# Performance work log

Hardware: AMD Instinct MI355X
Metric: run time of the kernel (lower is better)

The kernel has to match this reference:

```python
import jax, jax.numpy as jnp
import numpy as np

D_MODEL = 1024
D_FF = 4 * D_MODEL
NUM_TILES = 8
B, T = 4, 2048


def setup_inputs() -> dict:
    key = jax.random.key(0)
    ks = jax.random.split(key, 7)
    s = 0.02
    return {
        "x": jax.random.normal(ks[0], (B, T, D_MODEL), dtype=jnp.float32),
        "gate_W": jax.random.normal(ks[1], (D_MODEL, NUM_TILES), dtype=jnp.float32) * s,
        "gate_b": jnp.zeros((NUM_TILES,), dtype=jnp.float32),
        "up_W": jax.random.normal(ks[2], (NUM_TILES, D_MODEL, D_FF), dtype=jnp.float32) * s,
        "up_b": jnp.zeros((NUM_TILES, D_FF), dtype=jnp.float32),
        "down_W": jax.random.normal(ks[3], (NUM_TILES, D_FF, D_MODEL), dtype=jnp.float32) * s,
        "down_b": jnp.zeros((NUM_TILES, D_MODEL), dtype=jnp.float32),
    }


def top1_gate(logits):
    # Hard one-hot of argmax; straight-through identity gradient (Top1Gate).
    hard = jax.nn.one_hot(jnp.argmax(logits, axis=-1), logits.shape[-1], dtype=logits.dtype)
    return hard + (logits - jax.lax.stop_gradient(logits))


def trix_linear(x, gate, W, b):
    # x: [N, I], gate: [N, E] one-hot, W: [E, I, O], b: [E, O]
    # Per-tile linear combined by gate weight; loop over small fixed E.
    out = jnp.zeros((x.shape[0], W.shape[2]), dtype=x.dtype)
    for e in range(W.shape[0]):
        out = out + gate[:, e:e + 1] * (x @ W[e] + b[e])
    return out


def reference(x, gate_W, gate_b, up_W, up_b, down_W, down_b):
    Bv, Tv, C = x.shape
    xf = x.reshape(Bv * Tv, C)                      # [N, C]
    gate = top1_gate(xf @ gate_W + gate_b)          # [N, E]
    h = jax.nn.relu(trix_linear(xf, gate, up_W, up_b))   # [N, 4C]
    # dropout in eval mode (identity)
    out = trix_linear(h, gate, down_W, down_b)      # [N, C]
    return out.reshape(Bv, Tv, C), gate.reshape(Bv, Tv, -1)
```

## Files before the change

### kernel.cpp

```cpp
#include <hip/hip_runtime.h>
#include <hip/hip_bf16.h>
#include <stdint.h>

#define NTOK 8192
#define DM   1024
#define DFF  4096
#define NE   8

typedef __bf16 bf16x8 __attribute__((ext_vector_type(8)));
typedef short  short8 __attribute__((ext_vector_type(8)));
typedef float  floatx4 __attribute__((ext_vector_type(4)));

#define WS_CNT   0
#define WS_OFF   64
#define WS_EIDX  1024
#define WS_PERM  (WS_EIDX + NTOK * 4)
#define WS_XPERM (WS_PERM + NTOK * 4)
#define WS_HPERM (WS_XPERM + (NTOK + 128) * DM * 2)

__device__ __forceinline__ unsigned short f2bf(float f) {
  union { float f; unsigned u; } v; v.f = f;
  return (unsigned short)((v.u + 0x7FFFu + ((v.u >> 16) & 1u)) >> 16);
}

__device__ __forceinline__ float f4get(const float4& v, int i) {
  return i == 0 ? v.x : i == 1 ? v.y : i == 2 ? v.z : v.w;
}

__global__ __launch_bounds__(256) void gate_kernel(
    const float* __restrict__ x, const float* __restrict__ gW,
    const float* __restrict__ gb, float* __restrict__ gate_out,
    int* __restrict__ eidx) {
  int wave = threadIdx.x >> 6;
  int lane = threadIdx.x & 63;
  int t = blockIdx.x * 4 + wave;
  const float4* xr = (const float4*)(x + (size_t)t * DM + lane * 16);
  float acc[8] = {0, 0, 0, 0, 0, 0, 0, 0};
#pragma unroll
  for (int q = 0; q < 4; ++q) {
    float4 xv = xr[q];
    int kbase = lane * 16 + q * 4;
#pragma unroll
    for (int d = 0; d < 4; ++d) {
      float xs = f4get(xv, d);
      const float4* g4 = (const float4*)(gW + (size_t)(kbase + d) * NE);
      float4 g0 = g4[0], g1 = g4[1];
      acc[0] += xs * g0.x; acc[1] += xs * g0.y;
      acc[2] += xs * g0.z; acc[3] += xs * g0.w;
      acc[4] += xs * g1.x; acc[5] += xs * g1.y;
      acc[6] += xs * g1.z; acc[7] += xs * g1.w;
    }
  }
#pragma unroll
  for (int off = 32; off > 0; off >>= 1) {
#pragma unroll
    for (int e = 0; e < 8; ++e) acc[e] += __shfl_down(acc[e], off);
  }
  if (lane == 0) {
    float best = acc[0] + gb[0];
    int bi = 0;
#pragma unroll
    for (int e = 1; e < 8; ++e) {
      float v = acc[e] + gb[e];
      if (v > best) { best = v; bi = e; }
    }
#pragma unroll
    for (int e = 0; e < 8; ++e) gate_out[(size_t)t * NE + e] = (e == bi) ? 1.0f : 0.0f;
    eidx[t] = bi;
  }
}

__global__ __launch_bounds__(1024) void rank_kernel(
    const int* __restrict__ eidx, int* __restrict__ counts,
    int* __restrict__ offs, int* __restrict__ perm) {
  __shared__ unsigned long long sa[1024], sb[1024];
  int tid = threadIdx.x;
  int e8[8];
  unsigned long long ca = 0, cb = 0;
#pragma unroll
  for (int j = 0; j < 8; ++j) {
    int e = eidx[tid * 8 + j];
    e8[j] = e;
    if (e < 4) ca += 1ull << (16 * e);
    else       cb += 1ull << (16 * (e - 4));
  }
  sa[tid] = ca; sb[tid] = cb;
  __syncthreads();
  for (int off = 1; off < 1024; off <<= 1) {
    unsigned long long ta = 0, tb = 0;
    if (tid >= off) { ta = sa[tid - off]; tb = sb[tid - off]; }
    __syncthreads();
    sa[tid] += ta; sb[tid] += tb;
    __syncthreads();
  }
  unsigned long long tot_a = sa[1023], tot_b = sb[1023];
  int cnt_e[8];
#pragma unroll
  for (int e = 0; e < 4; ++e) cnt_e[e] = (int)((tot_a >> (16 * e)) & 0xFFFF);
#pragma unroll
  for (int e = 0; e < 4; ++e) cnt_e[e + 4] = (int)((tot_b >> (16 * e)) & 0xFFFF);
  int off_e[8]; int s = 0;
#pragma unroll
  for (int e = 0; e < 8; ++e) { off_e[e] = s; s += cnt_e[e]; }
  if (tid < 8) { counts[tid] = cnt_e[tid]; offs[tid] = off_e[tid]; }
  unsigned long long ia = sa[tid] - ca, ib = sb[tid] - cb;
  int run[8];
#pragma unroll
  for (int e = 0; e < 4; ++e) run[e] = (int)((ia >> (16 * e)) & 0xFFFF);
#pragma unroll
  for (int e = 0; e < 4; ++e) run[e + 4] = (int)((ib >> (16 * e)) & 0xFFFF);
#pragma unroll
  for (int j = 0; j < 8; ++j) {
    int e = e8[j];
    int pos = off_e[e] + run[e]++;
    perm[pos] = tid * 8 + j;
  }
}

__global__ __launch_bounds__(256) void scatter_data_kernel(
    const float* __restrict__ x, const int* __restrict__ perm,
    unsigned short* __restrict__ xperm) {
  int wave = threadIdx.x >> 6, lane = threadIdx.x & 63;
  int p = blockIdx.x * 4 + wave;
  int t = perm[p];
  const float4* xr = (const float4*)(x + (size_t)t * DM);
#pragma unroll
  for (int q = 0; q < 4; ++q) {
    float4 v = xr[q * 64 + lane];
    uint2 pk;
    pk.x = (unsigned)f2bf(v.x) | ((unsigned)f2bf(v.y) << 16);
    pk.y = (unsigned)f2bf(v.z) | ((unsigned)f2bf(v.w) << 16);
    *(uint2*)(xperm + (size_t)p * DM + q * 256 + lane * 4) = pk;
  }
}

__global__ __launch_bounds__(256) void up_gemm_kernel(
    const unsigned short* __restrict__ xperm,
    const float* __restrict__ upW, const float* __restrict__ upB,
    const int* __restrict__ counts, const int* __restrict__ offs,
    unsigned short* __restrict__ hperm) {
  int e = blockIdx.y >> 6;
  int mt = blockIdx.y & 63;
  int cnt = counts[e];
  if (mt * 128 >= cnt) return;
  int row0 = offs[e] + mt * 128;
  int rows_valid = cnt - mt * 128; if (rows_valid > 128) rows_valid = 128;
  int n0 = blockIdx.x * 128;
  const float* Bg = upW + (size_t)e * DM * DFF;

  __shared__ unsigned short sA[128 * 40];
  __shared__ unsigned short sB[128 * 40];

  int tid = threadIdx.x;
  int wave = tid >> 6, lane = tid & 63;
  int wm = (wave >> 1) * 64, wn = (wave & 1) * 64;

  floatx4 acc[4][4];
#pragma unroll
  for (int i = 0; i < 4; ++i)
#pragma unroll
    for (int j = 0; j < 4; ++j) acc[i][j] = (floatx4){0.f, 0.f, 0.f, 0.f};

  int ar = tid >> 2;
  int ac = (tid & 3) * 8;
  int nq = (tid & 31) * 4;
  int kq = (tid >> 5) * 4;

  for (int k0 = 0; k0 < DM; k0 += 32) {
    __syncthreads();
#pragma unroll
    for (int p = 0; p < 2; ++p) {
      int r = p * 64 + ar;
      short8 av = *(const short8*)(xperm + (size_t)(row0 + r) * DM + k0 + ac);
      *(short8*)(sA + r * 40 + ac) = av;
    }
    float4 bv[4];
#pragma unroll
    for (int dk = 0; dk < 4; ++dk)
      bv[dk] = *(const float4*)(Bg + (size_t)(k0 + kq + dk) * DFF + n0 + nq);
#pragma unroll
    for (int dn = 0; dn < 4; ++dn) {
      uint2 pk;
      pk.x = (unsigned)f2bf(f4get(bv[0], dn)) | ((unsigned)f2bf(f4get(bv[1], dn)) << 16);
      pk.y = (unsigned)f2bf(f4get(bv[2], dn)) | ((unsigned)f2bf(f4get(bv[3], dn)) << 16);
      *(uint2*)(sB + (nq + dn) * 40 + kq) = pk;
    }
    __syncthreads();
    bf16x8 a[4], b[4];
#pragma unroll
    for (int i = 0; i < 4; ++i)
      a[i] = *(const bf16x8*)(sA + (wm + i * 16 + (lane & 15)) * 40 + (lane >> 4) * 8);
#pragma unroll
    for (int j = 0; j < 4; ++j)
      b[j] = *(const bf16x8*)(sB + (wn + j * 16 + (lane & 15)) * 40 + (lane >> 4) * 8);
#pragma unroll
    for (int i = 0; i < 4; ++i)
#pragma unroll
      for (int j = 0; j < 4; ++j)
        acc[i][j] = __builtin_amdgcn_mfma_f32_16x16x32_bf16(a[i], b[j], acc[i][j], 0, 0, 0);
  }

  const float* ub = upB + (size_t)e * DFF;
#pragma unroll
  for (int i = 0; i < 4; ++i) {
#pragma unroll
    for (int r = 0; r < 4; ++r) {
      int rl = wm + i * 16 + (lane >> 4) * 4 + r;
      if (rl < rows_valid) {
        size_t rowg = (size_t)(row0 + rl) * DFF;
#pragma unroll
        for (int j = 0; j < 4; ++j) {
          int col = n0 + wn + j * 16 + (lane & 15);
          float v = acc[i][j][r] + ub[col];
          v = v > 0.f ? v : 0.f;
          hperm[rowg + col] = f2bf(v);
        }
      }
    }
  }
}

__global__ __launch_bounds__(256) void down_gemm_kernel(
    const unsigned short* __restrict__ hperm,
    const float* __restrict__ dW, const float* __restrict__ dB,
    const int* __restrict__ counts, const int* __restrict__ offs,
    const int* __restrict__ perm, float* __restrict__ out) {
  int e = blockIdx.y >> 6;
  int mt = blockIdx.y & 63;
  int cnt = counts[e];
  if (mt * 128 >= cnt) return;
  int row0 = offs[e] + mt * 128;
  int rows_valid = cnt - mt * 128; if (rows_valid > 128) rows_valid = 128;
  int n0 = blockIdx.x * 128;
  const float* Bg = dW + (size_t)e * DFF * DM;

  __shared__ unsigned short sA[128 * 40];
  __shared__ unsigned short sB[128 * 40];

  int tid = threadIdx.x;
  int wave = tid >> 6, lane = tid & 63;
  int wm = (wave >> 1) * 64, wn = (wave & 1) * 64;

  floatx4 acc[4][4];
#pragma unroll
  for (int i = 0; i < 4; ++i)
#pragma unroll
    for (int j = 0; j < 4; ++j) acc[i][j] = (floatx4){0.f, 0.f, 0.f, 0.f};

  int ar = tid >> 2;
  int ac = (tid & 3) * 8;
  int nq = (tid & 31) * 4;
  int kq = (tid >> 5) * 4;

  for (int k0 = 0; k0 < DFF; k0 += 32) {
    __syncthreads();
#pragma unroll
    for (int p = 0; p < 2; ++p) {
      int r = p * 64 + ar;
      short8 av = *(const short8*)(hperm + (size_t)(row0 + r) * DFF + k0 + ac);
      *(short8*)(sA + r * 40 + ac) = av;
    }
    float4 bv[4];
#pragma unroll
    for (int dk = 0; dk < 4; ++dk)
      bv[dk] = *(const float4*)(Bg + (size_t)(k0 + kq + dk) * DM + n0 + nq);
#pragma unroll
    for (int dn = 0; dn < 4; ++dn) {
      uint2 pk;
      pk.x = (unsigned)f2bf(f4get(bv[0], dn)) | ((unsigned)f2bf(f4get(bv[1], dn)) << 16);
      pk.y = (unsigned)f2bf(f4get(bv[2], dn)) | ((unsigned)f2bf(f4get(bv[3], dn)) << 16);
      *(uint2*)(sB + (nq + dn) * 40 + kq) = pk;
    }
    __syncthreads();
    bf16x8 a[4], b[4];
#pragma unroll
    for (int i = 0; i < 4; ++i)
      a[i] = *(const bf16x8*)(sA + (wm + i * 16 + (lane & 15)) * 40 + (lane >> 4) * 8);
#pragma unroll
    for (int j = 0; j < 4; ++j)
      b[j] = *(const bf16x8*)(sB + (wn + j * 16 + (lane & 15)) * 40 + (lane >> 4) * 8);
#pragma unroll
    for (int i = 0; i < 4; ++i)
#pragma unroll
      for (int j = 0; j < 4; ++j)
        acc[i][j] = __builtin_amdgcn_mfma_f32_16x16x32_bf16(a[i], b[j], acc[i][j], 0, 0, 0);
  }

  const float* db = dB + (size_t)e * DM;
#pragma unroll
  for (int i = 0; i < 4; ++i) {
#pragma unroll
    for (int r = 0; r < 4; ++r) {
      int rl = wm + i * 16 + (lane >> 4) * 4 + r;
      if (rl < rows_valid) {
        int token = perm[row0 + rl];
        size_t og = (size_t)token * DM;
#pragma unroll
        for (int j = 0; j < 4; ++j) {
          int col = n0 + wn + j * 16 + (lane & 15);
          out[og + col] = acc[i][j][r] + db[col];
        }
      }
    }
  }
}

extern "C" void kernel_launch(void* const* d_in, const int* in_sizes, int n_in,
                              void* d_out, int out_size, void* d_ws, size_t ws_size,
                              hipStream_t stream) {
  const float* x   = (const float*)d_in[0];
  const float* gW  = (const float*)d_in[1];
  const float* gb  = (const float*)d_in[2];
  const float* upW = (const float*)d_in[3];
  const float* upB = (const float*)d_in[4];
  const float* dW  = (const float*)d_in[5];
  const float* dB  = (const float*)d_in[6];
  float* out      = (float*)d_out;
  float* gate_out = out + (size_t)NTOK * DM;

  char* ws = (char*)d_ws;
  int* cnt  = (int*)(ws + WS_CNT);
  int* off  = (int*)(ws + WS_OFF);
  int* eidx = (int*)(ws + WS_EIDX);
  int* perm = (int*)(ws + WS_PERM);
  unsigned short* xperm = (unsigned short*)(ws + WS_XPERM);
  unsigned short* hperm = (unsigned short*)(ws + WS_HPERM);

  gate_kernel<<<NTOK / 4, 256, 0, stream>>>(x, gW, gb, gate_out, eidx);
  rank_kernel<<<1, 1024, 0, stream>>>(eidx, cnt, off, perm);
  scatter_data_kernel<<<NTOK / 4, 256, 0, stream>>>(x, perm, xperm);
  up_gemm_kernel<<<dim3(DFF / 128, NE * 64), 256, 0, stream>>>(xperm, upW, upB, cnt, off, hperm);
  down_gemm_kernel<<<dim3(DM / 128, NE * 64), 256, 0, stream>>>(hperm, dW, dB, cnt, off, perm, out);
}
```

Before: 671.4 us.

## Pre-convert weights to transposed bf16 and use direct global-to-LDS loads

Adds a conversion kernel that casts the up and down weights to bf16 once per call and transposes them to K-contiguous layout in workspace. The GEMMs then fill shared memory with global_load_lds 16-byte transfers instead of loading fp32 and converting in registers, and drop the padded LDS stride. A 1D grid remap interleaves workgroups across XCDs. This adds a full weight read and write pass each call, and the unpadded LDS layout may cause bank conflicts on the MFMA operand reads.

```diff
diff --git a/kernel.cpp b/kernel.cpp
--- a/kernel.cpp
+++ b/kernel.cpp
@@ -16,7 +16,9 @@
 #define WS_EIDX  1024
 #define WS_PERM  (WS_EIDX + NTOK * 4)
 #define WS_XPERM (WS_PERM + NTOK * 4)
-#define WS_HPERM (WS_XPERM + (NTOK + 128) * DM * 2)
+#define WS_HPERM (WS_XPERM + (size_t)(NTOK + 128) * DM * 2)
+#define WS_UPWT  (WS_HPERM + (size_t)(NTOK + 128) * DFF * 2)
+#define WS_DWT   (WS_UPWT + (size_t)NE * DM * DFF * 2)
 
 __device__ __forceinline__ unsigned short f2bf(float f) {
   union { float f; unsigned u; } v; v.f = f;
@@ -25,6 +27,38 @@
 
 __device__ __forceinline__ float f4get(const float4& v, int i) {
   return i == 0 ? v.x : i == 1 ? v.y : i == 2 ? v.z : v.w;
+}
+
+__device__ __forceinline__ void gload_lds16(const void* g, void* l) {
+  __builtin_amdgcn_global_load_lds(
+      (const __attribute__((address_space(1))) unsigned int*)g,
+      (__attribute__((address_space(3))) unsigned int*)l, 16, 0, 0);
+}
+
+__global__ __launch_bounds__(256) void wconv_kernel(
+    const float* __restrict__ W, unsigned short* __restrict__ Wt,
+    int K, int N) {
+  __shared__ __attribute__((aligned(16))) unsigned short s[64][72];
+  int n0 = blockIdx.x * 64;
+  int k0 = blockIdx.y * 64;
+  const float* Wp = W + (size_t)blockIdx.z * K * N + (size_t)k0 * N + n0;
+  int t = threadIdx.x;
+  int kr = t >> 4;
+  int nc = (t & 15) * 4;
+#pragma unroll
+  for (int q = 0; q < 4; ++q) {
+    float4 v = *(const float4*)(Wp + (size_t)(q * 16 + kr) * N + nc);
+    s[nc + 0][q * 16 + kr] = f2bf(v.x);
+    s[nc + 1][q * 16 + kr] = f2bf(v.y);
+    s[nc + 2][q * 16 + kr] = f2bf(v.z);
+    s[nc + 3][q * 16 + kr] = f2bf(v.w);
+  }
+  __syncthreads();
+  int nr = t >> 2;
+  int kc = (t & 3) * 16;
+  unsigned short* dst = Wt + (size_t)blockIdx.z * N * K + (size_t)(n0 + nr) * K + k0 + kc;
+  *(uint4*)dst       = *(const uint4*)&s[nr][kc];
+  *(uint4*)(dst + 8) = *(const uint4*)&s[nr][kc + 8];
 }
 
 __global__ __launch_bounds__(256) void gate_kernel(
@@ -136,63 +170,61 @@
 
 __global__ __launch_bounds__(256) void up_gemm_kernel(
     const unsigned short* __restrict__ xperm,
-    const float* __restrict__ upW, const float* __restrict__ upB,
+    const unsigned short* __restrict__ upWt,
+    const float* __restrict__ upB,
     const int* __restrict__ counts, const int* __restrict__ offs,
     unsigned short* __restrict__ hperm) {
-  int e = blockIdx.y >> 6;
-  int mt = blockIdx.y & 63;
+  const int nwg = NE * 32 * 64;
+  int orig = blockIdx.x;
+  int wg = (orig & 7) * (nwg >> 3) + (orig >> 3);
+  int e  = wg >> 11;
+  int r  = wg & 2047;
+  int nt = r >> 6;
+  int mt = r & 63;
   int cnt = counts[e];
   if (mt * 128 >= cnt) return;
   int row0 = offs[e] + mt * 128;
   int rows_valid = cnt - mt * 128; if (rows_valid > 128) rows_valid = 128;
-  int n0 = blockIdx.x * 128;
-  const float* Bg = upW + (size_t)e * DM * DFF;
-
-  __shared__ unsigned short sA[128 * 40];
-  __shared__ unsigned short sB[128 * 40];
+  int n0 = nt * 128;
+
+  __shared__ __attribute__((aligned(16))) unsigned short sA[128 * 32];
+  __shared__ __attribute__((aligned(16))) unsigned short sB[128 * 32];
 
   int tid = threadIdx.x;
   int wave = tid >> 6, lane = tid & 63;
   int wm = (wave >> 1) * 64, wn = (wave & 1) * 64;
 
+  int srow = wave * 32 + (lane >> 2);
+  int scol = (lane & 3) * 8;
+  const unsigned short* gA0 = xperm + (size_t)(row0 + srow) * DM + scol;
+  const unsigned short* gA1 = gA0 + 16 * DM;
+  const unsigned short* gB0 = upWt + (size_t)e * DFF * DM + (size_t)(n0 + srow) * DM + scol;
+  const unsigned short* gB1 = gB0 + 16 * DM;
+  unsigned short* lA0 = sA + wave * 1024;
+  unsigned short* lA1 = lA0 + 512;
+  unsigned short* lB0 = sB + wave * 1024;
+  unsigned short* lB1 = lB0 + 512;
+
   floatx4 acc[4][4];
 #pragma unroll
   for (int i = 0; i < 4; ++i)
 #pragma unroll
     for (int j = 0; j < 4; ++j) acc[i][j] = (floatx4){0.f, 0.f, 0.f, 0.f};
 
-  int ar = tid >> 2;
-  int ac = (tid & 3) * 8;
-  int nq = (tid & 31) * 4;
-  int kq = (tid >> 5) * 4;
-
   for (int k0 = 0; k0 < DM; k0 += 32) {
     __syncthreads();
-#pragma unroll
-    for (int p = 0; p < 2; ++p) {
-      int r = p * 64 + ar;
-      short8 av = *(const short8*)(xperm + (size_t)(row0 + r) * DM + k0 + ac);
-      *(short8*)(sA + r * 40 + ac) = av;
-    }
-    float4 bv[4];
-#pragma unroll
-    for (int dk = 0; dk < 4; ++dk)
-      bv[dk] = *(const float4*)(Bg + (size_t)(k0 + kq + dk) * DFF + n0 + nq);
-#pragma unroll
-    for (int dn = 0; dn < 4; ++dn) {
-      uint2 pk;
-      pk.x = (unsigned)f2bf(f4get(bv[0], dn)) | ((unsigned)f2bf(f4get(bv[1], dn)) << 16);
-      pk.y = (unsigned)f2bf(f4get(bv[2], dn)) | ((unsigned)f2bf(f4get(bv[3], dn)) << 16);
-      *(uint2*)(sB + (nq + dn) * 40 + kq) = pk;
-    }
+    gload_lds16(gA0 + k0, lA0);
+    gload_lds16(gA1 + k0, lA1);
+    gload_lds16(gB0 + k0, lB0);
+    gload_lds16(gB1 + k0, lB1);
     __syncthreads();
     bf16x8 a[4], b[4];
 #pragma unroll
     for (int i = 0; i < 4; ++i)
-      a[i] = *(const bf16x8*)(sA + (wm + i * 16 + (lane & 15)) * 40 + (lane >> 4) * 8);
+      a[i] = *(const bf16x8*)(sA + (wm + i * 16 + (lane & 15)) * 32 + (lane >> 4) * 8);
 #pragma unroll
     for (int j = 0; j < 4; ++j)
-      b[j] = *(const bf16x8*)(sB + (wn + j * 16 + (lane & 15)) * 40 + (lane >> 4) * 8);
+      b[j] = *(const bf16x8*)(sB + (wn + j * 16 + (lane & 15)) * 32 + (lane >> 4) * 8);
 #pragma unroll
     for (int i = 0; i < 4; ++i)
 #pragma unroll
@@ -204,14 +236,14 @@
 #pragma unroll
   for (int i = 0; i < 4; ++i) {
 #pragma unroll
-    for (int r = 0; r < 4; ++r) {
-      int rl = wm + i * 16 + (lane >> 4) * 4 + r;
+    for (int r2 = 0; r2 < 4; ++r2) {
+      int rl = wm + i * 16 + (lane >> 4) * 4 + r2;
       if (rl < rows_valid) {
         size_t rowg = (size_t)(row0 + rl) * DFF;
 #pragma unroll
         for (int j = 0; j < 4; ++j) {
           int col = n0 + wn + j * 16 + (lane & 15);
-          float v = acc[i][j][r] + ub[col];
+          float v = acc[i][j][r2] + ub[col];
           v = v > 0.f ? v : 0.f;
           hperm[rowg + col] = f2bf(v);
         }
@@ -222,63 +254,61 @@
 
 __global__ __launch_bounds__(256) void down_gemm_kernel(
     const unsigned short* __restrict__ hperm,
-    const float* __restrict__ dW, const float* __restrict__ dB,
+    const unsigned short* __restrict__ dWt,
+    const float* __restrict__ dB,
     const int* __restrict__ counts, const int* __restrict__ offs,
     const int* __restrict__ perm, float* __restrict__ out) {
-  int e = blockIdx.y >> 6;
-  int mt = blockIdx.y & 63;
+  const int nwg = NE * 8 * 64;
+  int orig = blockIdx.x;
+  int wg = (orig & 7) * (nwg >> 3) + (orig >> 3);
+  int e  = wg >> 9;
+  int r  = wg & 511;
+  int nt = r >> 6;
+  int mt = r & 63;
   int cnt = counts[e];
   if (mt * 128 >= cnt) return;
   int row0 = offs[e] + mt * 128;
   int rows_valid = cnt - mt * 128; if (rows_valid > 128) rows_valid = 128;
-  int n0 = blockIdx.x * 128;
-  const float* Bg = dW + (size_t)e * DFF * DM;
-
-  __shared__ unsigned short sA[128 * 40];
-  __shared__ unsigned short sB[128 * 40];
+  int n0 = nt * 128;
+
+  __shared__ __attribute__((aligned(16))) unsigned short sA[128 * 32];
+  __shared__ __attribute__((aligned(16))) unsigned short sB[128 * 32];
 
   int tid = threadIdx.x;
   int wave = tid >> 6, lane = tid & 63;
   int wm = (wave >> 1) * 64, wn = (wave & 1) * 64;
 
+  int srow = wave * 32 + (lane >> 2);
+  int scol = (lane & 3) * 8;
+  const unsigned short* gA0 = hperm + (size_t)(row0 + srow) * DFF + scol;
+  const unsigned short* gA1 = gA0 + 16 * DFF;
+  const unsigned short* gB0 = dWt + (size_t)e * DM * DFF + (size_t)(n0 + srow) * DFF + scol;
+  const unsigned short* gB1 = gB0 + 16 * DFF;
+  unsigned short* lA0 = sA + wave * 1024;
+  unsigned short* lA1 = lA0 + 512;
+  unsigned short* lB0 = sB + wave * 1024;
+  unsigned short* lB1 = lB0 + 512;
+
   floatx4 acc[4][4];
 #pragma unroll
   for (int i = 0; i < 4; ++i)
 #pragma unroll
     for (int j = 0; j < 4; ++j) acc[i][j] = (floatx4){0.f, 0.f, 0.f, 0.f};
 
-  int ar = tid >> 2;
-  int ac = (tid & 3) * 8;
-  int nq = (tid & 31) * 4;
-  int kq = (tid >> 5) * 4;
-
   for (int k0 = 0; k0 < DFF; k0 += 32) {
     __syncthreads();
-#pragma unroll
-    for (int p = 0; p < 2; ++p) {
-      int r = p * 64 + ar;
-      short8 av = *(const short8*)(hperm + (size_t)(row0 + r) * DFF + k0 + ac);
-      *(short8*)(sA + r * 40 + ac) = av;
-    }
-    float4 bv[4];
-#pragma unroll
-    for (int dk = 0; dk < 4; ++dk)
-      bv[dk] = *(const float4*)(Bg + (size_t)(k0 + kq + dk) * DM + n0 + nq);
-#pragma unroll
-    for (int dn = 0; dn < 4; ++dn) {
-      uint2 pk;
-      pk.x = (unsigned)f2bf(f4get(bv[0], dn)) | ((unsigned)f2bf(f4get(bv[1], dn)) << 16);
-      pk.y = (unsigned)f2bf(f4get(bv[2], dn)) | ((unsigned)f2bf(f4get(bv[3], dn)) << 16);
-      *(uint2*)(sB + (nq + dn) * 40 + kq) = pk;
-    }
+    gload_lds16(gA0 + k0, lA0);
+    gload_lds16(gA1 + k0, lA1);
+    gload_lds16(gB0 + k0, lB0);
+    gload_lds16(gB1 + k0, lB1);
     __syncthreads();
     bf16x8 a[4], b[4];
 #pragma unroll
     for (int i = 0; i < 4; ++i)
-      a[i] = *(const bf16x8*)(sA + (wm + i * 16 + (lane & 15)) * 40 + (lane >> 4) * 8);
+      a[i] = *(const bf16x8*)(sA + (wm + i * 16 + (lane & 15)) * 32 + (lane >> 4) * 8);
 #pragma unroll
     for (int j = 0; j < 4; ++j)
-      b[j] = *(const bf16x8*)(sB + (wn + j * 16 + (lane & 15)) * 40 + (lane >> 4) * 8);
+      b[j] = *(const bf16x8*)(sB + (wn + j * 16 + (lane & 15)) * 32 + (lane >> 4) * 8);
 #pragma unroll
     for (int i = 0; i < 4; ++i)
 #pragma unroll
@@ -290,15 +320,15 @@
 #pragma unroll
   for (int i = 0; i < 4; ++i) {
 #pragma unroll
-    for (int r = 0; r < 4; ++r) {
-      int rl = wm + i * 16 + (lane >> 4) * 4 + r;
+    for (int r2 = 0; r2 < 4; ++r2) {
+      int rl = wm + i * 16 + (lane >> 4) * 4 + r2;
       if (rl < rows_valid) {
         int token = perm[row0 + rl];
         size_t og = (size_t)token * DM;
 #pragma unroll
         for (int j = 0; j < 4; ++j) {
           int col = n0 + wn + j * 16 + (lane & 15);
-          out[og + col] = acc[i][j][r] + db[col];
+          out[og + col] = acc[i][j][r2] + db[col];
         }
       }
     }
@@ -325,10 +355,15 @@
   int* perm = (int*)(ws + WS_PERM);
   unsigned short* xperm = (unsigned short*)(ws + WS_XPERM);
   unsigned short* hperm = (unsigned short*)(ws + WS_HPERM);
+  unsigned short* upWt  = (unsigned short*)(ws + WS_UPWT);
+  unsigned short* dWt   = (unsigned short*)(ws + WS_DWT);
+
+  wconv_kernel<<<dim3(DFF / 64, DM / 64, NE), 256, 0, stream>>>(upW, upWt, DM, DFF);
+  wconv_kernel<<<dim3(DM / 64, DFF / 64, NE), 256, 0, stream>>>(dW, dWt, DFF, DM);
 
   gate_kernel<<<NTOK / 4, 256, 0, stream>>>(x, gW, gb, gate_out, eidx);
   rank_kernel<<<1, 1024, 0, stream>>>(eidx, cnt, off, perm);
   scatter_data_kernel<<<NTOK / 4, 256, 0, stream>>>(x, perm, xperm);
-  up_gemm_kernel<<<dim3(DFF / 128, NE * 64), 256, 0, stream>>>(xperm, upW, upB, cnt, off, hperm);
-  down_gemm_kernel<<<dim3(DM / 128, NE * 64), 256, 0, stream>>>(hperm, dW, dB, cnt, off, perm, out);
-}
+  up_gemm_kernel<<<NE * 32 * 64, 256, 0, stream>>>(xperm, upWt, upB, cnt, off, hperm);
+  down_gemm_kernel<<<NE * 8 * 64, 256, 0, stream>>>(hperm, dWt, dB, cnt, off, perm, out);
+}
```

After: 626.6 us. 1.07x faster.
